# Kernel tuning notes

Hardware: AMD Instinct MI355X
Metric: run time of the kernel (lower is better)

The kernel has to match this reference:

```python
import jax, jax.numpy as jnp
import numpy as np
from jax.ops import segment_sum, segment_max, segment_min

N_NODES = 200000
N_HE = 100000     # number of hyperedges (nets)
NNZ = 1000000     # number of pins (node,hyperedge) incidences
F_RAW = 29        # raw node features; +2 fake_pos +1 ismacro = 32 = num_features
PIN_D = 4
C = 64            # nhid (heads = 1)
N_MACRO = 512
NUM_CLASSES = 1
SLOPE = 0.1


def _lrelu(v):
    return jnp.where(v >= 0, v, SLOPE * v)


def setup_inputs() -> dict:
    key = jax.random.key(0)
    ks = jax.random.split(key, 16)
    x = jax.random.normal(ks[0], (N_NODES, F_RAW), jnp.float32)
    fake_pos = jax.random.uniform(ks[1], (N_NODES, 2), dtype=jnp.float32)
    node_idx = jax.random.randint(ks[2], (NNZ,), 0, N_NODES)
    he_idx = jax.random.randint(ks[3], (NNZ,), 0, N_HE)
    edge_index = jnp.stack([node_idx, he_idx]).astype(jnp.int32)
    pin_feature = jax.random.normal(ks[4], (NNZ, PIN_D), jnp.float32)
    macro_index = jax.random.randint(ks[5], (N_MACRO,), 0, N_NODES).astype(jnp.int32)
    F_IN = F_RAW + 3

    def lin(k, fi, fo):
        return (jax.random.normal(k, (fi, fo), jnp.float32) / np.float32(np.sqrt(fi)))

    W1 = lin(ks[6], F_IN, C); b1 = jnp.zeros((C,), jnp.float32)
    Wpin = lin(ks[7], PIN_D, C)
    att = jax.random.normal(ks[8], (2 * C,), jnp.float32) / np.float32(np.sqrt(2 * C))
    Wpost = lin(ks[9], 4 * C, C); bpost = jnp.zeros((C,), jnp.float32)
    Wm1 = lin(ks[10], 2 * C, C); bm1 = jnp.zeros((C,), jnp.float32)
    Wm2 = lin(ks[11], C, C // 2); bm2 = jnp.zeros((C // 2,), jnp.float32)
    Wm3 = lin(ks[12], C // 2, NUM_CLASSES); bm3 = jnp.zeros((NUM_CLASSES,), jnp.float32)
    return dict(x=x, fake_pos=fake_pos, edge_index=edge_index, pin_feature=pin_feature,
                macro_index=macro_index, W1=W1, b1=b1, Wpin=Wpin, att=att,
                Wpost=Wpost, bpost=bpost, Wm1=Wm1, bm1=bm1, Wm2=Wm2, bm2=bm2,
                Wm3=Wm3, bm3=bm3)


def _forward(x, fake_pos, edge_index, pin_feature, macro_index,
             W1, b1, Wpin, att, Wpost, bpost, Wm1, bm1, Wm2, bm2, Wm3, bm3):
    node_idx = edge_index[0]
    he_idx = edge_index[1]

    ismacro = jnp.zeros((N_NODES, 1), x.dtype).at[macro_index].set(1.0)
    h = jnp.concatenate([x, fake_pos, ismacro], axis=-1)  # (N, 32)

    xl = h @ W1 + b1                                      # (N, C) node embedding
    pin_m = pin_feature @ Wpin                            # (NNZ, C) pin embedding

    # node -> hyperedge aggregation (mean over incident pins)
    msg_ne = xl[node_idx] + pin_m                         # (NNZ, C)
    deg_e = segment_sum(jnp.ones((NNZ,), x.dtype), he_idx, num_segments=N_HE)
    e_feat = segment_sum(msg_ne, he_idx, num_segments=N_HE) / jnp.maximum(deg_e, 1.0)[:, None]

    # attention over incident hyperedges, softmax per node
    e_g = e_feat[he_idx]                                  # (NNZ, C)
    a_raw = _lrelu(jnp.concatenate([xl[node_idx], e_g], axis=-1) @ att)  # (NNZ,)
    m = segment_max(a_raw, node_idx, num_segments=N_NODES)
    m = jnp.where(jnp.isfinite(m), m, 0.0)
    ex = jnp.exp(a_raw - m[node_idx])
    den = segment_sum(ex, node_idx, num_segments=N_NODES)
    alpha = ex / (den[node_idx] + 1e-16)

    # hyperedge -> node: PNA multi-aggregation of attention-weighted messages
    msg = e_g * alpha[:, None]                            # (NNZ, C)
    deg_n = segment_sum(jnp.ones((NNZ,), x.dtype), node_idx, num_segments=N_NODES)
    deg_c = jnp.maximum(deg_n, 1.0)[:, None]
    s = segment_sum(msg, node_idx, num_segments=N_NODES)
    mean = s / deg_c
    mx = segment_max(msg, node_idx, num_segments=N_NODES)
    mx = jnp.where(deg_n[:, None] > 0, mx, 0.0)
    mn = segment_min(msg, node_idx, num_segments=N_NODES)
    mn = jnp.where(deg_n[:, None] > 0, mn, 0.0)
    sq = segment_sum(msg * msg, node_idx, num_segments=N_NODES) / deg_c
    std = jnp.sqrt(jnp.maximum(sq - mean * mean, 0.0) + 1e-12)

    pna = jnp.concatenate([mean, mx, mn, std], axis=-1) @ Wpost + bpost  # (N, C)
    hx = _lrelu(pna)

    # masked global-mean pools (single graph: batch is all zeros)
    pooled = jnp.concatenate([hx[macro_index].mean(0), hx.mean(0)])[None, :]  # (1, 2C)

    z = _lrelu(pooled @ Wm1 + bm1)
    z = _lrelu(z @ Wm2 + bm2)
    return z @ Wm3 + bm3                                  # (1, num_classes)


def reference(x, fake_pos, edge_index, pin_feature, macro_index,
              W1, b1, Wpin, att, Wpost, bpost, Wm1, bm1, Wm2, bm2, Wm3, bm3):
    return _forward(x, fake_pos, edge_index, pin_feature, macro_index,
                    W1, b1, Wpin, att, Wpost, bpost, Wm1, bm1, Wm2, bm2, Wm3, bm3)
```

## Files before the change

### kernel.cpp

```cpp
#include <hip/hip_runtime.h>
#include <math.h>

#define N_NODES 200000
#define N_HE    100000
#define NNZ     1000000
#define F_RAW   29
#define N_MACRO 512
#define SLOPE   0.1f
#define L_TOTAL (N_NODES + N_HE)
#define NB_SCAN 293

typedef __attribute__((ext_vector_type(8))) short bf16x8;
typedef __attribute__((ext_vector_type(4))) float f32x4;

__device__ __forceinline__ float lrelu(float v) { return v >= 0.f ? v : SLOPE * v; }
__device__ __forceinline__ float bf2f(unsigned short u) { return __uint_as_float(((unsigned)u) << 16); }
__device__ __forceinline__ unsigned short f2bf(float f) {
    unsigned u = __float_as_uint(f);
    unsigned r = u + 0x7FFFu + ((u >> 16) & 1u);
    return (unsigned short)(r >> 16);
}
__device__ __forceinline__ float bflo(unsigned u) { return __uint_as_float(u << 16); }
__device__ __forceinline__ float bfhi(unsigned u) { return __uint_as_float(u & 0xffff0000u); }

__global__ __launch_bounds__(256) void fill_f32(float* p, long long n, float v) {
    long long i = (long long)blockIdx.x * blockDim.x + threadIdx.x;
    long long st = (long long)gridDim.x * blockDim.x;
    for (; i < n; i += st) p[i] = v;
}

__global__ __launch_bounds__(256) void k_pre(
    const int* __restrict__ mi, float* __restrict__ ismacro, int* __restrict__ mcount,
    const float* __restrict__ W1, const float* __restrict__ b1,
    const float* __restrict__ att, float* __restrict__ va,
    const int* __restrict__ nidx, const int* __restrict__ hidx,
    int* __restrict__ cnt, int* __restrict__ rank_n, int* __restrict__ rank_e)
{
    if (blockIdx.x == 0) {
        int t = threadIdx.x;
        if (t < 32) {
            float a = 0.f;
            for (int c = 0; c < 64; c++) a += W1[t * 64 + c] * att[c];
            va[t] = a;
        } else if (t == 32) {
            float a = 0.f;
            for (int c = 0; c < 64; c++) a += b1[c] * att[c];
            va[32] = a;
        }
    } else if (blockIdx.x <= 2) {
        int i = (blockIdx.x - 1) * 256 + threadIdx.x;
        if (i < N_MACRO) {
            ismacro[mi[i]] = 1.0f;
            atomicAdd(&mcount[mi[i]], 1);
        }
    } else {
        int i = (blockIdx.x - 3) * 256 + threadIdx.x;
        int st = (gridDim.x - 3) * 256;
        for (int p = i; p < NNZ; p += st) {
            rank_n[p] = atomicAdd(&cnt[nidx[p]], 1);
            rank_e[p] = atomicAdd(&cnt[N_NODES + hidx[p]], 1);
        }
    }
}

__global__ __launch_bounds__(256) void k_scan1(const int* __restrict__ cnt,
                                               int* __restrict__ row_ptr, int* __restrict__ partials)
{
    __shared__ int sA[256], sB[256];
    const int t = threadIdx.x;
    const int base = blockIdx.x * 1024 + t * 4;
    int v0 = base + 0 < L_TOTAL ? cnt[base + 0] : 0;
    int v1 = base + 1 < L_TOTAL ? cnt[base + 1] : 0;
    int v2 = base + 2 < L_TOTAL ? cnt[base + 2] : 0;
    int v3 = base + 3 < L_TOTAL ? cnt[base + 3] : 0;
    sA[t] = v0 + v1 + v2 + v3;
    __syncthreads();
    int* src = sA; int* dst = sB;
    for (int off = 1; off < 256; off <<= 1) {
        int v = src[t];
        if (t >= off) v += src[t - off];
        dst[t] = v;
        __syncthreads();
        int* tmp = src; src = dst; dst = tmp;
    }
    int excl = t > 0 ? src[t - 1] : 0;
    if (base + 0 < L_TOTAL) row_ptr[base + 0] = excl;
    if (base + 1 < L_TOTAL) row_ptr[base + 1] = excl + v0;
    if (base + 2 < L_TOTAL) row_ptr[base + 2] = excl + v0 + v1;
    if (base + 3 < L_TOTAL) row_ptr[base + 3] = excl + v0 + v1 + v2;
    if (t == 255) partials[blockIdx.x] = src[255];
}

__global__ __launch_bounds__(512) void k_scan2(int* __restrict__ partials)
{
    __shared__ int sA[512], sB[512];
    const int t = threadIdx.x;
    sA[t] = t < NB_SCAN ? partials[t] : 0;
    __syncthreads();
    int* src = sA; int* dst = sB;
    for (int off = 1; off < 512; off <<= 1) {
        int v = src[t];
        if (t >= off) v += src[t - off];
        dst[t] = v;
        __syncthreads();
        int* tmp = src; src = dst; dst = tmp;
    }
    if (t < NB_SCAN) partials[t] = t > 0 ? src[t - 1] : 0;
    if (t == 0) partials[NB_SCAN] = src[511];
}

__global__ __launch_bounds__(256) void k_scan3(int* __restrict__ row_ptr, const int* __restrict__ partials)
{
    const int base = blockIdx.x * 1024 + threadIdx.x * 4;
    int add = partials[blockIdx.x];
    #pragma unroll
    for (int k = 0; k < 4; k++)
        if (base + k < L_TOTAL) row_ptr[base + k] += add;
    if (blockIdx.x == 0 && threadIdx.x == 0) row_ptr[L_TOTAL] = partials[NB_SCAN];
}

__global__ __launch_bounds__(256) void k_mid(
    const int* __restrict__ nidx, const int* __restrict__ hidx,
    const int* __restrict__ row_ptr,
    const int* __restrict__ rank_n, const int* __restrict__ rank_e,
    const float4* __restrict__ pf4, int* __restrict__ csr_n, int4* __restrict__ rec,
    const float* __restrict__ x, const float* __restrict__ fp,
    const float* __restrict__ ismacro, const float* __restrict__ va,
    unsigned short* __restrict__ h, float* __restrict__ xn_att)
{
    if (blockIdx.x < 2048) {
        int i = blockIdx.x * 256 + threadIdx.x;
        int st = 2048 * 256;
        for (int p = i; p < NNZ; p += st) {
            int n = nidx[p], e = hidx[p];
            csr_n[row_ptr[n] + rank_n[p]] = e;
            int pe = row_ptr[N_NODES + e] + rank_e[p];
            float4 q = pf4[p];
            int4 r;
            r.x = n;
            r.y = (int)((unsigned)f2bf(q.x) | ((unsigned)f2bf(q.y) << 16));
            r.z = (int)((unsigned)f2bf(q.z) | ((unsigned)f2bf(q.w) << 16));
            r.w = 0;
            rec[pe - NNZ] = r;
        }
    } else {
        const int lane = threadIdx.x & 63;
        const int half = lane >> 5, k = lane & 31;
        int wid = ((blockIdx.x - 2048) * 256 + threadIdx.x) >> 6;
        int nw = (1024 * 256) >> 6;
        float vak = va[k];
        float c0 = va[32];
        for (int base = wid * 2; base < N_NODES; base += nw * 2) {
            int n = base + half;
            float v;
            if (k < 29)       v = x[(size_t)n * F_RAW + k];
            else if (k == 29) v = fp[2 * n];
            else if (k == 30) v = fp[2 * n + 1];
            else              v = ismacro[n];
            h[(size_t)n * 32 + k] = f2bf(v);
            float r = v * vak;
            #pragma unroll
            for (int o = 16; o > 0; o >>= 1) r += __shfl_xor(r, o, 32);
            if (k == 0) xn_att[n] = r + c0;
        }
    }
}

__global__ __launch_bounds__(256) void k_he_agg(
    const int* __restrict__ row_ptr, const int4* __restrict__ rec,
    const float* __restrict__ W1, const float* __restrict__ Wpin,
    const float* __restrict__ b1, const float* __restrict__ att,
    const unsigned short* __restrict__ h,
    unsigned short* __restrict__ e_feat, float* __restrict__ e_att)
{
    __shared__ float sW1[32 * 64];
    __shared__ float sWp[4 * 64];
    __shared__ float sb1[64];
    for (int i = threadIdx.x; i < 32 * 64; i += 256) sW1[i] = W1[i];
    for (int i = threadIdx.x; i < 4 * 64; i += 256) sWp[i] = Wpin[i];
    if (threadIdx.x < 64) sb1[threadIdx.x] = b1[threadIdx.x];
    __syncthreads();
    const int lane = threadIdx.x & 63;
    const int g  = lane >> 3;
    const int gl = lane & 7;
    float att2 = att[64 + lane];
    int wid = (blockIdx.x * blockDim.x + threadIdx.x) >> 6;
    int nw = (gridDim.x * blockDim.x) >> 6;
    for (int e = wid; e < N_HE; e += nw) {
        int start = row_ptr[N_NODES + e];
        int deg = row_ptr[N_NODES + e + 1] - start;
        float h0 = 0.f, h1 = 0.f, h2 = 0.f, h3 = 0.f;
        float pa = 0.f, pb = 0.f;
        const int4* rbase = rec + (start - NNZ);
        int t = g;
        for (; t + 8 < deg; t += 16) {
            int4 rA = rbase[t];
            int4 rB = rbase[t + 8];
            ushort4 uA = *(const ushort4*)&h[(size_t)rA.x * 32 + 4 * gl];
            ushort4 uB = *(const ushort4*)&h[(size_t)rB.x * 32 + 4 * gl];
            h0 += bf2f(uA.x) + bf2f(uB.x);
            h1 += bf2f(uA.y) + bf2f(uB.y);
            h2 += bf2f(uA.z) + bf2f(uB.z);
            h3 += bf2f(uA.w) + bf2f(uB.w);
            unsigned pyA = (gl == 0) ? (unsigned)rA.y : ((gl == 1) ? (unsigned)rA.z : 0u);
            unsigned pyB = (gl == 0) ? (unsigned)rB.y : ((gl == 1) ? (unsigned)rB.z : 0u);
            pa += bflo(pyA) + bflo(pyB);
            pb += bfhi(pyA) + bfhi(pyB);
        }
        if (t < deg) {
            int4 r = rbase[t];
            ushort4 u = *(const ushort4*)&h[(size_t)r.x * 32 + 4 * gl];
            h0 += bf2f(u.x); h1 += bf2f(u.y); h2 += bf2f(u.z); h3 += bf2f(u.w);
            unsigned py = (gl == 0) ? (unsigned)r.y : ((gl == 1) ? (unsigned)r.z : 0u);
            pa += bflo(py); pb += bfhi(py);
        }
        #pragma unroll
        for (int o = 8; o <= 32; o <<= 1) {
            h0 += __shfl_xor(h0, o); h1 += __shfl_xor(h1, o);
            h2 += __shfl_xor(h2, o); h3 += __shfl_xor(h3, o);
            pa += __shfl_xor(pa, o); pb += __shfl_xor(pb, o);
        }
        float p0 = __shfl(pa, 0, 64), p1 = __shfl(pb, 0, 64);
        float p2 = __shfl(pa, 1, 64), p3 = __shfl(pb, 1, 64);
        float acc = (float)deg * sb1[lane]
                  + p0 * sWp[lane] + p1 * sWp[64 + lane]
                  + p2 * sWp[128 + lane] + p3 * sWp[192 + lane];
        #pragma unroll
        for (int kk = 0; kk < 8; kk++) {
            float a0 = __shfl(h0, kk, 64), a1 = __shfl(h1, kk, 64);
            float a2 = __shfl(h2, kk, 64), a3 = __shfl(h3, kk, 64);
            acc += a0 * sW1[(4 * kk + 0) * 64 + lane] + a1 * sW1[(4 * kk + 1) * 64 + lane]
                 + a2 * sW1[(4 * kk + 2) * 64 + lane] + a3 * sW1[(4 * kk + 3) * 64 + lane];
        }
        float d = (float)(deg > 0 ? deg : 1);
        float v = acc / d;
        e_feat[(size_t)e * 64 + lane] = f2bf(v);
        float r = v * att2;
        #pragma unroll
        for (int o = 32; o > 0; o >>= 1) r += __shfl_down(r, o, 64);
        if (lane == 0) e_att[e] = r;
    }
}

__global__ __launch_bounds__(256, 4) void k_fused(
    const int* __restrict__ row_ptr, const int* __restrict__ csr,
    const float* __restrict__ xn_att, const float* __restrict__ e_att,
    const unsigned short* __restrict__ e_feat,
    const float* __restrict__ Wpost, const float* __restrict__ bpost,
    const int* __restrict__ mcount,
    float* __restrict__ sum_all, float* __restrict__ sum_mac)
{
    __shared__ __align__(16) unsigned short scat[16 * 264];
    const int lane = threadIdx.x & 63;
    const int wave = threadIdx.x >> 6;
    const int half = lane >> 5;
    const int c2   = lane & 31;
    const int quad = lane >> 4;
    const int nn   = lane & 15;
    bf16x8 wfrag[8];
    #pragma unroll
    for (int s = 0; s < 8; s++) {
        bf16x8 w;
        #pragma unroll
        for (int j = 0; j < 8; j++)
            w[j] = (short)f2bf(Wpost[(size_t)(32 * s + quad * 8 + j) * 64 + wave * 16 + nn]);
        wfrag[s] = w;
    }
    float bias = bpost[wave * 16 + nn];
    float pool = 0.f, pmac = 0.f;
    const int nbatches = N_NODES / 16;
    for (int b = blockIdx.x; b < nbatches; b += gridDim.x) {
        const int base = b * 16;
        __syncthreads();
        for (int i = 0; i < 4; i++) {
            int j = wave * 4 + i;
            int n = base + j;
            int start = row_ptr[n];
            int deg = row_ptr[n + 1] - start;
            float xn = xn_att[n];
            float sw = 0.f;
            float sx = 0.f, sy = 0.f, qx = 0.f, qy = 0.f;
            float mxx = -INFINITY, mxy = -INFINITY, mnx = INFINITY, mny = INFINITY;
            int t = half;
            for (; t + 2 < deg; t += 4) {
                int e0 = csr[start + t];
                int e1 = csr[start + t + 2];
                float w0 = __expf(lrelu(xn + e_att[e0]));
                float w1 = __expf(lrelu(xn + e_att[e1]));
                unsigned u0 = ((const unsigned*)&e_feat[(size_t)e0 * 64])[c2];
                unsigned u1 = ((const unsigned*)&e_feat[(size_t)e1 * 64])[c2];
                float v0x = bflo(u0) * w0, v0y = bfhi(u0) * w0;
                float v1x = bflo(u1) * w1, v1y = bfhi(u1) * w1;
                sw += w0 + w1;
                sx += v0x + v1x; sy += v0y + v1y;
                qx += v0x * v0x + v1x * v1x; qy += v0y * v0y + v1y * v1y;
                mxx = fmaxf(mxx, fmaxf(v0x, v1x)); mxy = fmaxf(mxy, fmaxf(v0y, v1y));
                mnx = fminf(mnx, fminf(v0x, v1x)); mny = fminf(mny, fminf(v0y, v1y));
            }
            for (; t < deg; t += 2) {
                int e = csr[start + t];
                float w = __expf(lrelu(xn + e_att[e]));
                unsigned u = ((const unsigned*)&e_feat[(size_t)e * 64])[c2];
                float vx = bflo(u) * w, vy = bfhi(u) * w;
                sw += w; sx += vx; sy += vy; qx += vx * vx; qy += vy * vy;
                mxx = fmaxf(mxx, vx); mxy = fmaxf(mxy, vy);
                mnx = fminf(mnx, vx); mny = fminf(mny, vy);
            }
            sw  += __shfl_xor(sw, 32);
            sx  += __shfl_xor(sx, 32);  sy += __shfl_xor(sy, 32);
            qx  += __shfl_xor(qx, 32);  qy += __shfl_xor(qy, 32);
            mxx = fmaxf(mxx, __shfl_xor(mxx, 32)); mxy = fmaxf(mxy, __shfl_xor(mxy, 32));
            mnx = fminf(mnx, __shfl_xor(mnx, 32)); mny = fminf(mny, __shfl_xor(mny, 32));
            float invD = 1.f / (sw + 1e-16f);
            float dc = (float)(deg > 0 ? deg : 1);
            float meanx = sx * invD / dc, meany = sy * invD / dc;
            float sqmx = qx * invD * invD / dc, sqmy = qy * invD * invD / dc;
            float stdx = sqrtf(fmaxf(sqmx - meanx * meanx, 0.f) + 1e-12f);
            float stdy = sqrtf(fmaxf(sqmy - meany * meany, 0.f) + 1e-12f);
            ushort2* row = (ushort2*)&scat[j * 264];
            if (half == 0) {
                ushort2 a; a.x = f2bf(meanx); a.y = f2bf(meany);
                row[c2] = a;
                ushort2 bmax; bmax.x = f2bf(deg > 0 ? mxx * invD : 0.f);
                bmax.y = f2bf(deg > 0 ? mxy * invD : 0.f);
                row[32 + c2] = bmax;
            } else {
                ushort2 bmin; bmin.x = f2bf(deg > 0 ? mnx * invD : 0.f);
                bmin.y = f2bf(deg > 0 ? mny * invD : 0.f);
                row[64 + c2] = bmin;
                ushort2 bstd; bstd.x = f2bf(stdx); bstd.y = f2bf(stdy);
                row[96 + c2] = bstd;
            }
        }
        __syncthreads();
        f32x4 acc = {0.f, 0.f, 0.f, 0.f};
        #pragma unroll
        for (int s = 0; s < 8; s++) {
            bf16x8 a = *(const bf16x8*)&scat[nn * 264 + 32 * s + quad * 8];
            acc = __builtin_amdgcn_mfma_f32_16x16x32_bf16(a, wfrag[s], acc, 0, 0, 0);
        }
        int4 mc4 = *(const int4*)&mcount[base + 4 * quad];
        float h0 = lrelu(acc[0] + bias);
        float h1 = lrelu(acc[1] + bias);
        float h2 = lrelu(acc[2] + bias);
        float h3 = lrelu(acc[3] + bias);
        pool += h0 + h1 + h2 + h3;
        pmac += (float)mc4.x * h0 + (float)mc4.y * h1 + (float)mc4.z * h2 + (float)mc4.w * h3;
    }
    pool += __shfl_xor(pool, 16); pool += __shfl_xor(pool, 32);
    pmac += __shfl_xor(pmac, 16); pmac += __shfl_xor(pmac, 32);
    if (quad == 0) {
        atomicAdd(&sum_all[wave * 16 + nn], pool);
        atomicAdd(&sum_mac[wave * 16 + nn], pmac);
    }
}

__global__ __launch_bounds__(256) void k_final(
    const float* __restrict__ sum_all, const float* __restrict__ sum_mac,
    const float* __restrict__ Wm1, const float* __restrict__ bm1,
    const float* __restrict__ Wm2, const float* __restrict__ bm2,
    const float* __restrict__ Wm3, const float* __restrict__ bm3,
    float* __restrict__ out)
{
    __shared__ float spool[128];
    __shared__ float z1[64];
    __shared__ float z2[32];
    if (threadIdx.x < 64) {
        spool[threadIdx.x]      = sum_mac[threadIdx.x] / (float)N_MACRO;
        spool[64 + threadIdx.x] = sum_all[threadIdx.x] / (float)N_NODES;
    }
    __syncthreads();
    if (threadIdx.x < 64) {
        int j = threadIdx.x;
        float a = bm1[j];
        #pragma unroll 4
        for (int k = 0; k < 128; k++) a += spool[k] * Wm1[k * 64 + j];
        z1[j] = lrelu(a);
    }
    __syncthreads();
    if (threadIdx.x < 32) {
        int j = threadIdx.x;
        float a = bm2[j];
        #pragma unroll 4
        for (int k = 0; k < 64; k++) a += z1[k] * Wm2[k * 32 + j];
        z2[j] = lrelu(a);
    }
    __syncthreads();
    if (threadIdx.x == 0) {
        float a = bm3[0];
        #pragma unroll
        for (int k = 0; k < 32; k++) a += z2[k] * Wm3[k];
        out[0] = a;
    }
}

extern "C" void kernel_launch(void* const* d_in, const int* in_sizes, int n_in,
                              void* d_out, int out_size, void* d_ws, size_t ws_size,
                              hipStream_t stream)
{
    const float* x        = (const float*)d_in[0];
    const float* fake_pos = (const float*)d_in[1];
    const int*   edge     = (const int*)d_in[2];
    const float* pinf     = (const float*)d_in[3];
    const int*   macro    = (const int*)d_in[4];
    const float* W1    = (const float*)d_in[5];
    const float* b1    = (const float*)d_in[6];
    const float* Wpin  = (const float*)d_in[7];
    const float* att   = (const float*)d_in[8];
    const float* Wpost = (const float*)d_in[9];
    const float* bpost = (const float*)d_in[10];
    const float* Wm1   = (const float*)d_in[11];
    const float* bm1   = (const float*)d_in[12];
    const float* Wm2   = (const float*)d_in[13];
    const float* bm2   = (const float*)d_in[14];
    const float* Wm3   = (const float*)d_in[15];
    const float* bm3   = (const float*)d_in[16];
    float* out = (float*)d_out;

    float* ws = (float*)d_ws;
    float*    ismacro = ws;
    float*    sum_all = ws + 200000;
    float*    sum_mac = ws + 200064;
    int*      mcount  = (int*)(ws + 200128);
    int*      cnt     = (int*)(ws + 400128);
    int*      row_ptr  = (int*)(ws + 700128);
    int*      partials = (int*)(ws + 1000132);
    float*    va       = ws + 1000432;
    int*      rank_n   = (int*)(ws + 1000472);
    int*      rank_e   = (int*)(ws + 2000472);
    int*      csr_n    = (int*)(ws + 3000472);
    int4*     rec      = (int4*)(ws + 4000472);
    float*    e_att    = ws + 8000472;
    float*    xn_att   = ws + 8100472;
    unsigned short* h      = (unsigned short*)(ws + 8300472);
    unsigned short* e_feat = (unsigned short*)(ws + 11500472);

    const int* nidx = edge;
    const int* hidx = edge + NNZ;

    fill_f32<<<1024, 256, 0, stream>>>(ws, 700128LL, 0.f);
    k_pre<<<2051, 256, 0, stream>>>(macro, ismacro, mcount, W1, b1, att, va,
                                    nidx, hidx, cnt, rank_n, rank_e);
    k_scan1<<<NB_SCAN, 256, 0, stream>>>(cnt, row_ptr, partials);
    k_scan2<<<1, 512, 0, stream>>>(partials);
    k_scan3<<<NB_SCAN, 256, 0, stream>>>(row_ptr, partials);
    k_mid<<<3072, 256, 0, stream>>>(nidx, hidx, row_ptr, rank_n, rank_e,
                                    (const float4*)pinf, csr_n, rec,
                                    x, fake_pos, ismacro, va, h, xn_att);
    k_he_agg<<<2048, 256, 0, stream>>>(row_ptr, rec, W1, Wpin, b1, att, h, e_feat, e_att);
    k_fused<<<2048, 256, 0, stream>>>(row_ptr, csr_n, xn_att, e_att, e_feat, Wpost, bpost,
                                      mcount, sum_all, sum_mac);
    k_final<<<1, 256, 0, stream>>>(sum_all, sum_mac, Wm1, bm1, Wm2, bm2, Wm3, bm3, out);
}
```

Before: 474.0 us.

## Precompute per-pin attention weights and move h-build into the counting kernel

Adds a k_wt pass that computes each node-pin attention weight and the per-node softmax denominator once, storing (edge, weight) pairs. k_fused then reads these pairs instead of recomputing the exp per lane and gathering e_att. The h/xn_att build moves from the scatter kernel into the atomic counting kernel, so it overlaps with the atomics instead of the scatter. In exchange, k_wt is a one-thread-per-node serial loop with extra writes of an 8 MB wrec array.

```diff
diff --git a/kernel.cpp b/kernel.cpp
--- a/kernel.cpp
+++ b/kernel.cpp
@@ -29,12 +29,10 @@
     for (; i < n; i += st) p[i] = v;
 }
 
-__global__ __launch_bounds__(256) void k_pre(
+__global__ __launch_bounds__(256) void k_tiny(
     const int* __restrict__ mi, float* __restrict__ ismacro, int* __restrict__ mcount,
     const float* __restrict__ W1, const float* __restrict__ b1,
-    const float* __restrict__ att, float* __restrict__ va,
-    const int* __restrict__ nidx, const int* __restrict__ hidx,
-    int* __restrict__ cnt, int* __restrict__ rank_n, int* __restrict__ rank_e)
+    const float* __restrict__ att, float* __restrict__ va)
 {
     if (blockIdx.x == 0) {
         int t = threadIdx.x;
@@ -47,83 +45,18 @@
             for (int c = 0; c < 64; c++) a += b1[c] * att[c];
             va[32] = a;
         }
-    } else if (blockIdx.x <= 2) {
+    } else {
         int i = (blockIdx.x - 1) * 256 + threadIdx.x;
         if (i < N_MACRO) {
             ismacro[mi[i]] = 1.0f;
             atomicAdd(&mcount[mi[i]], 1);
         }
-    } else {
-        int i = (blockIdx.x - 3) * 256 + threadIdx.x;
-        int st = (gridDim.x - 3) * 256;
-        for (int p = i; p < NNZ; p += st) {
-            rank_n[p] = atomicAdd(&cnt[nidx[p]], 1);
-            rank_e[p] = atomicAdd(&cnt[N_NODES + hidx[p]], 1);
-        }
-    }
-}
-
-__global__ __launch_bounds__(256) void k_scan1(const int* __restrict__ cnt,
-                                               int* __restrict__ row_ptr, int* __restrict__ partials)
-{
-    __shared__ int sA[256], sB[256];
-    const int t = threadIdx.x;
-    const int base = blockIdx.x * 1024 + t * 4;
-    int v0 = base + 0 < L_TOTAL ? cnt[base + 0] : 0;
-    int v1 = base + 1 < L_TOTAL ? cnt[base + 1] : 0;
-    int v2 = base + 2 < L_TOTAL ? cnt[base + 2] : 0;
-    int v3 = base + 3 < L_TOTAL ? cnt[base + 3] : 0;
-    sA[t] = v0 + v1 + v2 + v3;
-    __syncthreads();
-    int* src = sA; int* dst = sB;
-    for (int off = 1; off < 256; off <<= 1) {
-        int v = src[t];
-        if (t >= off) v += src[t - off];
-        dst[t] = v;
-        __syncthreads();
-        int* tmp = src; src = dst; dst = tmp;
-    }
-    int excl = t > 0 ? src[t - 1] : 0;
-    if (base + 0 < L_TOTAL) row_ptr[base + 0] = excl;
-    if (base + 1 < L_TOTAL) row_ptr[base + 1] = excl + v0;
-    if (base + 2 < L_TOTAL) row_ptr[base + 2] = excl + v0 + v1;
-    if (base + 3 < L_TOTAL) row_ptr[base + 3] = excl + v0 + v1 + v2;
-    if (t == 255) partials[blockIdx.x] = src[255];
-}
-
-__global__ __launch_bounds__(512) void k_scan2(int* __restrict__ partials)
-{
-    __shared__ int sA[512], sB[512];
-    const int t = threadIdx.x;
-    sA[t] = t < NB_SCAN ? partials[t] : 0;
-    __syncthreads();
-    int* src = sA; int* dst = sB;
-    for (int off = 1; off < 512; off <<= 1) {
-        int v = src[t];
-        if (t >= off) v += src[t - off];
-        dst[t] = v;
-        __syncthreads();
-        int* tmp = src; src = dst; dst = tmp;
-    }
-    if (t < NB_SCAN) partials[t] = t > 0 ? src[t - 1] : 0;
-    if (t == 0) partials[NB_SCAN] = src[511];
-}
-
-__global__ __launch_bounds__(256) void k_scan3(int* __restrict__ row_ptr, const int* __restrict__ partials)
-{
-    const int base = blockIdx.x * 1024 + threadIdx.x * 4;
-    int add = partials[blockIdx.x];
-    #pragma unroll
-    for (int k = 0; k < 4; k++)
-        if (base + k < L_TOTAL) row_ptr[base + k] += add;
-    if (blockIdx.x == 0 && threadIdx.x == 0) row_ptr[L_TOTAL] = partials[NB_SCAN];
-}
-
-__global__ __launch_bounds__(256) void k_mid(
+    }
+}
+
+__global__ __launch_bounds__(256) void k_cnt_h(
     const int* __restrict__ nidx, const int* __restrict__ hidx,
-    const int* __restrict__ row_ptr,
-    const int* __restrict__ rank_n, const int* __restrict__ rank_e,
-    const float4* __restrict__ pf4, int* __restrict__ csr_n, int4* __restrict__ rec,
+    int* __restrict__ cnt, int* __restrict__ rank_n, int* __restrict__ rank_e,
     const float* __restrict__ x, const float* __restrict__ fp,
     const float* __restrict__ ismacro, const float* __restrict__ va,
     unsigned short* __restrict__ h, float* __restrict__ xn_att)
@@ -132,16 +65,8 @@
         int i = blockIdx.x * 256 + threadIdx.x;
         int st = 2048 * 256;
         for (int p = i; p < NNZ; p += st) {
-            int n = nidx[p], e = hidx[p];
-            csr_n[row_ptr[n] + rank_n[p]] = e;
-            int pe = row_ptr[N_NODES + e] + rank_e[p];
-            float4 q = pf4[p];
-            int4 r;
-            r.x = n;
-            r.y = (int)((unsigned)f2bf(q.x) | ((unsigned)f2bf(q.y) << 16));
-            r.z = (int)((unsigned)f2bf(q.z) | ((unsigned)f2bf(q.w) << 16));
-            r.w = 0;
-            rec[pe - NNZ] = r;
+            rank_n[p] = atomicAdd(&cnt[nidx[p]], 1);
+            rank_e[p] = atomicAdd(&cnt[N_NODES + hidx[p]], 1);
         }
     } else {
         const int lane = threadIdx.x & 63;
@@ -163,6 +88,84 @@
             for (int o = 16; o > 0; o >>= 1) r += __shfl_xor(r, o, 32);
             if (k == 0) xn_att[n] = r + c0;
         }
+    }
+}
+
+__global__ __launch_bounds__(256) void k_scan1(const int* __restrict__ cnt,
+                                               int* __restrict__ row_ptr, int* __restrict__ partials)
+{
+    __shared__ int sA[256], sB[256];
+    const int t = threadIdx.x;
+    const int base = blockIdx.x * 1024 + t * 4;
+    int v0 = base + 0 < L_TOTAL ? cnt[base + 0] : 0;
+    int v1 = base + 1 < L_TOTAL ? cnt[base + 1] : 0;
+    int v2 = base + 2 < L_TOTAL ? cnt[base + 2] : 0;
+    int v3 = base + 3 < L_TOTAL ? cnt[base + 3] : 0;
+    sA[t] = v0 + v1 + v2 + v3;
+    __syncthreads();
+    int* src = sA; int* dst = sB;
+    for (int off = 1; off < 256; off <<= 1) {
+        int v = src[t];
+        if (t >= off) v += src[t - off];
+        dst[t] = v;
+        __syncthreads();
+        int* tmp = src; src = dst; dst = tmp;
+    }
+    int excl = t > 0 ? src[t - 1] : 0;
+    if (base + 0 < L_TOTAL) row_ptr[base + 0] = excl;
+    if (base + 1 < L_TOTAL) row_ptr[base + 1] = excl + v0;
+    if (base + 2 < L_TOTAL) row_ptr[base + 2] = excl + v0 + v1;
+    if (base + 3 < L_TOTAL) row_ptr[base + 3] = excl + v0 + v1 + v2;
+    if (t == 255) partials[blockIdx.x] = src[255];
+}
+
+__global__ __launch_bounds__(512) void k_scan2(int* __restrict__ partials)
+{
+    __shared__ int sA[512], sB[512];
+    const int t = threadIdx.x;
+    sA[t] = t < NB_SCAN ? partials[t] : 0;
+    __syncthreads();
+    int* src = sA; int* dst = sB;
+    for (int off = 1; off < 512; off <<= 1) {
+        int v = src[t];
+        if (t >= off) v += src[t - off];
+        dst[t] = v;
+        __syncthreads();
+        int* tmp = src; src = dst; dst = tmp;
+    }
+    if (t < NB_SCAN) partials[t] = t > 0 ? src[t - 1] : 0;
+    if (t == 0) partials[NB_SCAN] = src[511];
+}
+
+__global__ __launch_bounds__(256) void k_scan3(int* __restrict__ row_ptr, const int* __restrict__ partials)
+{
+    const int base = blockIdx.x * 1024 + threadIdx.x * 4;
+    int add = partials[blockIdx.x];
+    #pragma unroll
+    for (int k = 0; k < 4; k++)
+        if (base + k < L_TOTAL) row_ptr[base + k] += add;
+    if (blockIdx.x == 0 && threadIdx.x == 0) row_ptr[L_TOTAL] = partials[NB_SCAN];
+}
+
+__global__ __launch_bounds__(256) void k_scatter(
+    const int* __restrict__ nidx, const int* __restrict__ hidx,
+    const int* __restrict__ row_ptr,
+    const int* __restrict__ rank_n, const int* __restrict__ rank_e,
+    const float4* __restrict__ pf4, int* __restrict__ csr_n, int4* __restrict__ rec)
+{
+    int i = blockIdx.x * 256 + threadIdx.x;
+    int st = gridDim.x * 256;
+    for (int p = i; p < NNZ; p += st) {
+        int n = nidx[p], e = hidx[p];
+        csr_n[row_ptr[n] + rank_n[p]] = e;
+        int pe = row_ptr[N_NODES + e] + rank_e[p];
+        float4 q = pf4[p];
+        int4 r;
+        r.x = n;
+        r.y = (int)((unsigned)f2bf(q.x) | ((unsigned)f2bf(q.y) << 16));
+        r.z = (int)((unsigned)f2bf(q.z) | ((unsigned)f2bf(q.w) << 16));
+        r.w = 0;
+        rec[pe - NNZ] = r;
     }
 }
 
@@ -242,9 +245,32 @@
     }
 }
 
+__global__ __launch_bounds__(256) void k_wt(
+    const int* __restrict__ row_ptr, const int* __restrict__ csr_n,
+    const float* __restrict__ xn_att, const float* __restrict__ e_att,
+    int2* __restrict__ wrec, float* __restrict__ inv_den)
+{
+    int i = blockIdx.x * 256 + threadIdx.x;
+    int st = gridDim.x * 256;
+    for (int n = i; n < N_NODES; n += st) {
+        int start = row_ptr[n];
+        int deg = row_ptr[n + 1] - start;
+        float xn = xn_att[n];
+        float sw = 0.f;
+        for (int t = 0; t < deg; t++) {
+            int e = csr_n[start + t];
+            float w = __expf(lrelu(xn + e_att[e]));
+            sw += w;
+            int2 r; r.x = e; r.y = __float_as_int(w);
+            wrec[start + t] = r;
+        }
+        inv_den[n] = 1.f / (sw + 1e-16f);
+    }
+}
+
 __global__ __launch_bounds__(256, 4) void k_fused(
-    const int* __restrict__ row_ptr, const int* __restrict__ csr,
-    const float* __restrict__ xn_att, const float* __restrict__ e_att,
+    const int* __restrict__ row_ptr, const int2* __restrict__ wrec,
+    const float* __restrict__ inv_den, const float* __restrict__ e_att,
     const unsigned short* __restrict__ e_feat,
     const float* __restrict__ Wpost, const float* __restrict__ bpost,
     const int* __restrict__ mcount,
@@ -277,41 +303,38 @@
             int n = base + j;
             int start = row_ptr[n];
             int deg = row_ptr[n + 1] - start;
-            float xn = xn_att[n];
-            float sw = 0.f;
+            const int2* rb = wrec + start;
             float sx = 0.f, sy = 0.f, qx = 0.f, qy = 0.f;
             float mxx = -INFINITY, mxy = -INFINITY, mnx = INFINITY, mny = INFINITY;
             int t = half;
             for (; t + 2 < deg; t += 4) {
-                int e0 = csr[start + t];
-                int e1 = csr[start + t + 2];
-                float w0 = __expf(lrelu(xn + e_att[e0]));
-                float w1 = __expf(lrelu(xn + e_att[e1]));
-                unsigned u0 = ((const unsigned*)&e_feat[(size_t)e0 * 64])[c2];
-                unsigned u1 = ((const unsigned*)&e_feat[(size_t)e1 * 64])[c2];
+                int2 r0 = rb[t];
+                int2 r1 = rb[t + 2];
+                float w0 = __int_as_float(r0.y);
+                float w1 = __int_as_float(r1.y);
+                unsigned u0 = ((const unsigned*)&e_feat[(size_t)r0.x * 64])[c2];
+                unsigned u1 = ((const unsigned*)&e_feat[(size_t)r1.x * 64])[c2];
                 float v0x = bflo(u0) * w0, v0y = bfhi(u0) * w0;
                 float v1x = bflo(u1) * w1, v1y = bfhi(u1) * w1;
-                sw += w0 + w1;
                 sx += v0x + v1x; sy += v0y + v1y;
                 qx += v0x * v0x + v1x * v1x; qy += v0y * v0y + v1y * v1y;
                 mxx = fmaxf(mxx, fmaxf(v0x, v1x)); mxy = fmaxf(mxy, fmaxf(v0y, v1y));
                 mnx = fminf(mnx, fminf(v0x, v1x)); mny = fminf(mny, fminf(v0y, v1y));
             }
             for (; t < deg; t += 2) {
-                int e = csr[start + t];
-                float w = __expf(lrelu(xn + e_att[e]));
-                unsigned u = ((const unsigned*)&e_feat[(size_t)e * 64])[c2];
+                int2 r = rb[t];
+                float w = __int_as_float(r.y);
+                unsigned u = ((const unsigned*)&e_feat[(size_t)r.x * 64])[c2];
                 float vx = bflo(u) * w, vy = bfhi(u) * w;
-                sw += w; sx += vx; sy += vy; qx += vx * vx; qy += vy * vy;
+                sx += vx; sy += vy; qx += vx * vx; qy += vy * vy;
                 mxx = fmaxf(mxx, vx); mxy = fmaxf(mxy, vy);
                 mnx = fminf(mnx, vx); mny = fminf(mny, vy);
             }
-            sw  += __shfl_xor(sw, 32);
             sx  += __shfl_xor(sx, 32);  sy += __shfl_xor(sy, 32);
             qx  += __shfl_xor(qx, 32);  qy += __shfl_xor(qy, 32);
             mxx = fmaxf(mxx, __shfl_xor(mxx, 32)); mxy = fmaxf(mxy, __shfl_xor(mxy, 32));
             mnx = fminf(mnx, __shfl_xor(mnx, 32)); mny = fminf(mny, __shfl_xor(mny, 32));
-            float invD = 1.f / (sw + 1e-16f);
+            float invD = inv_den[n];
             float dc = (float)(deg > 0 ? deg : 1);
             float meanx = sx * invD / dc, meany = sy * invD / dc;
             float sqmx = qx * invD * invD / dc, sqmy = qy * invD * invD / dc;
@@ -430,25 +453,28 @@
     int*      rank_e   = (int*)(ws + 2000472);
     int*      csr_n    = (int*)(ws + 3000472);
     int4*     rec      = (int4*)(ws + 4000472);
-    float*    e_att    = ws + 8000472;
-    float*    xn_att   = ws + 8100472;
-    unsigned short* h      = (unsigned short*)(ws + 8300472);
-    unsigned short* e_feat = (unsigned short*)(ws + 11500472);
+    int2*     wrec     = (int2*)(ws + 8000472);
+    float*    inv_den  = ws + 10000472;
+    float*    e_att    = ws + 10200472;
+    float*    xn_att   = ws + 10300472;
+    unsigned short* h      = (unsigned short*)(ws + 10500472);
+    unsigned short* e_feat = (unsigned short*)(ws + 13700472);
 
     const int* nidx = edge;
     const int* hidx = edge + NNZ;
 
     fill_f32<<<1024, 256, 0, stream>>>(ws, 700128LL, 0.f);
-    k_pre<<<2051, 256, 0, stream>>>(macro, ismacro, mcount, W1, b1, att, va,
-                                    nidx, hidx, cnt, rank_n, rank_e);
+    k_tiny<<<3, 256, 0, stream>>>(macro, ismacro, mcount, W1, b1, att, va);
+    k_cnt_h<<<3072, 256, 0, stream>>>(nidx, hidx, cnt, rank_n, rank_e,
+                                      x, fake_pos, ismacro, va, h, xn_att);
     k_scan1<<<NB_SCAN, 256, 0, stream>>>(cnt, row_ptr, partials);
     k_scan2<<<1, 512, 0, stream>>>(partials);
     k_scan3<<<NB_SCAN, 256, 0, stream>>>(row_ptr, partials);
-    k_mid<<<3072, 256, 0, stream>>>(nidx, hidx, row_ptr, rank_n, rank_e,
-                                    (const float4*)pinf, csr_n, rec,
-                                    x, fake_pos, ismacro, va, h, xn_att);
+    k_scatter<<<2048, 256, 0, stream>>>(nidx, hidx, row_ptr, rank_n, rank_e,
+                                        (const float4*)pinf, csr_n, rec);
     k_he_agg<<<2048, 256, 0, stream>>>(row_ptr, rec, W1, Wpin, b1, att, h, e_feat, e_att);
-    k_fused<<<2048, 256, 0, stream>>>(row_ptr, csr_n, xn_att, e_att, e_feat, Wpost, bpost,
+    k_wt<<<782, 256, 0, stream>>>(row_ptr, csr_n, xn_att, e_att, wrec, inv_den);
+    k_fused<<<2048, 256, 0, stream>>>(row_ptr, wrec, inv_den, e_att, e_feat, Wpost, bpost,
                                       mcount, sum_all, sum_mac);
     k_final<<<1, 256, 0, stream>>>(sum_all, sum_mac, Wm1, bm1, Wm2, bm2, Wm3, bm3, out);
 }
```

After: 489.6 us. 3.3% more time.

## Regroup counting with node-feature prep and widen per-lane gather in node aggregation

Applied to the files above, without the earlier changes.

The node-feature packing and attention-score computation move out of the post-scan scatter kernel and into the same launch as the atomic counting pass, so the scatter kernel only builds the CSR and record arrays. The ismacro and va setup is split into a tiny separate kernel that runs first, since the feature packing now depends on it. In the node aggregation, each lane now handles four feature channels across quarter-wave slices of the neighbour list instead of two channels across half-waves. This gives wider ushort4 loads and a direct 8-byte store into the shared staging tile, at the cost of more accumulator registers and a two-step shuffle reduction.

```diff
diff --git a/kernel.cpp b/kernel.cpp
--- a/kernel.cpp
+++ b/kernel.cpp
@@ -29,12 +29,10 @@
     for (; i < n; i += st) p[i] = v;
 }
 
-__global__ __launch_bounds__(256) void k_pre(
+__global__ __launch_bounds__(256) void k_tiny(
     const int* __restrict__ mi, float* __restrict__ ismacro, int* __restrict__ mcount,
     const float* __restrict__ W1, const float* __restrict__ b1,
-    const float* __restrict__ att, float* __restrict__ va,
-    const int* __restrict__ nidx, const int* __restrict__ hidx,
-    int* __restrict__ cnt, int* __restrict__ rank_n, int* __restrict__ rank_e)
+    const float* __restrict__ att, float* __restrict__ va)
 {
     if (blockIdx.x == 0) {
         int t = threadIdx.x;
@@ -47,83 +45,18 @@
             for (int c = 0; c < 64; c++) a += b1[c] * att[c];
             va[32] = a;
         }
-    } else if (blockIdx.x <= 2) {
+    } else {
         int i = (blockIdx.x - 1) * 256 + threadIdx.x;
         if (i < N_MACRO) {
             ismacro[mi[i]] = 1.0f;
             atomicAdd(&mcount[mi[i]], 1);
         }
-    } else {
-        int i = (blockIdx.x - 3) * 256 + threadIdx.x;
-        int st = (gridDim.x - 3) * 256;
-        for (int p = i; p < NNZ; p += st) {
-            rank_n[p] = atomicAdd(&cnt[nidx[p]], 1);
-            rank_e[p] = atomicAdd(&cnt[N_NODES + hidx[p]], 1);
-        }
-    }
-}
-
-__global__ __launch_bounds__(256) void k_scan1(const int* __restrict__ cnt,
-                                               int* __restrict__ row_ptr, int* __restrict__ partials)
-{
-    __shared__ int sA[256], sB[256];
-    const int t = threadIdx.x;
-    const int base = blockIdx.x * 1024 + t * 4;
-    int v0 = base + 0 < L_TOTAL ? cnt[base + 0] : 0;
-    int v1 = base + 1 < L_TOTAL ? cnt[base + 1] : 0;
-    int v2 = base + 2 < L_TOTAL ? cnt[base + 2] : 0;
-    int v3 = base + 3 < L_TOTAL ? cnt[base + 3] : 0;
-    sA[t] = v0 + v1 + v2 + v3;
-    __syncthreads();
-    int* src = sA; int* dst = sB;
-    for (int off = 1; off < 256; off <<= 1) {
-        int v = src[t];
-        if (t >= off) v += src[t - off];
-        dst[t] = v;
-        __syncthreads();
-        int* tmp = src; src = dst; dst = tmp;
-    }
-    int excl = t > 0 ? src[t - 1] : 0;
-    if (base + 0 < L_TOTAL) row_ptr[base + 0] = excl;
-    if (base + 1 < L_TOTAL) row_ptr[base + 1] = excl + v0;
-    if (base + 2 < L_TOTAL) row_ptr[base + 2] = excl + v0 + v1;
-    if (base + 3 < L_TOTAL) row_ptr[base + 3] = excl + v0 + v1 + v2;
-    if (t == 255) partials[blockIdx.x] = src[255];
-}
-
-__global__ __launch_bounds__(512) void k_scan2(int* __restrict__ partials)
-{
-    __shared__ int sA[512], sB[512];
-    const int t = threadIdx.x;
-    sA[t] = t < NB_SCAN ? partials[t] : 0;
-    __syncthreads();
-    int* src = sA; int* dst = sB;
-    for (int off = 1; off < 512; off <<= 1) {
-        int v = src[t];
-        if (t >= off) v += src[t - off];
-        dst[t] = v;
-        __syncthreads();
-        int* tmp = src; src = dst; dst = tmp;
-    }
-    if (t < NB_SCAN) partials[t] = t > 0 ? src[t - 1] : 0;
-    if (t == 0) partials[NB_SCAN] = src[511];
-}
-
-__global__ __launch_bounds__(256) void k_scan3(int* __restrict__ row_ptr, const int* __restrict__ partials)
-{
-    const int base = blockIdx.x * 1024 + threadIdx.x * 4;
-    int add = partials[blockIdx.x];
-    #pragma unroll
-    for (int k = 0; k < 4; k++)
-        if (base + k < L_TOTAL) row_ptr[base + k] += add;
-    if (blockIdx.x == 0 && threadIdx.x == 0) row_ptr[L_TOTAL] = partials[NB_SCAN];
-}
-
-__global__ __launch_bounds__(256) void k_mid(
+    }
+}
+
+__global__ __launch_bounds__(256) void k_cnt_h(
     const int* __restrict__ nidx, const int* __restrict__ hidx,
-    const int* __restrict__ row_ptr,
-    const int* __restrict__ rank_n, const int* __restrict__ rank_e,
-    const float4* __restrict__ pf4, int* __restrict__ csr_n, int4* __restrict__ rec,
+    int* __restrict__ cnt, int* __restrict__ rank_n, int* __restrict__ rank_e,
     const float* __restrict__ x, const float* __restrict__ fp,
     const float* __restrict__ ismacro, const float* __restrict__ va,
     unsigned short* __restrict__ h, float* __restrict__ xn_att)
@@ -132,16 +65,8 @@
         int i = blockIdx.x * 256 + threadIdx.x;
         int st = 2048 * 256;
         for (int p = i; p < NNZ; p += st) {
-            int n = nidx[p], e = hidx[p];
-            csr_n[row_ptr[n] + rank_n[p]] = e;
-            int pe = row_ptr[N_NODES + e] + rank_e[p];
-            float4 q = pf4[p];
-            int4 r;
-            r.x = n;
-            r.y = (int)((unsigned)f2bf(q.x) | ((unsigned)f2bf(q.y) << 16));
-            r.z = (int)((unsigned)f2bf(q.z) | ((unsigned)f2bf(q.w) << 16));
-            r.w = 0;
-            rec[pe - NNZ] = r;
+            rank_n[p] = atomicAdd(&cnt[nidx[p]], 1);
+            rank_e[p] = atomicAdd(&cnt[N_NODES + hidx[p]], 1);
         }
     } else {
         const int lane = threadIdx.x & 63;
@@ -163,6 +88,84 @@
             for (int o = 16; o > 0; o >>= 1) r += __shfl_xor(r, o, 32);
             if (k == 0) xn_att[n] = r + c0;
         }
+    }
+}
+
+__global__ __launch_bounds__(256) void k_scan1(const int* __restrict__ cnt,
+                                               int* __restrict__ row_ptr, int* __restrict__ partials)
+{
+    __shared__ int sA[256], sB[256];
+    const int t = threadIdx.x;
+    const int base = blockIdx.x * 1024 + t * 4;
+    int v0 = base + 0 < L_TOTAL ? cnt[base + 0] : 0;
+    int v1 = base + 1 < L_TOTAL ? cnt[base + 1] : 0;
+    int v2 = base + 2 < L_TOTAL ? cnt[base + 2] : 0;
+    int v3 = base + 3 < L_TOTAL ? cnt[base + 3] : 0;
+    sA[t] = v0 + v1 + v2 + v3;
+    __syncthreads();
+    int* src = sA; int* dst = sB;
+    for (int off = 1; off < 256; off <<= 1) {
+        int v = src[t];
+        if (t >= off) v += src[t - off];
+        dst[t] = v;
+        __syncthreads();
+        int* tmp = src; src = dst; dst = tmp;
+    }
+    int excl = t > 0 ? src[t - 1] : 0;
+    if (base + 0 < L_TOTAL) row_ptr[base + 0] = excl;
+    if (base + 1 < L_TOTAL) row_ptr[base + 1] = excl + v0;
+    if (base + 2 < L_TOTAL) row_ptr[base + 2] = excl + v0 + v1;
+    if (base + 3 < L_TOTAL) row_ptr[base + 3] = excl + v0 + v1 + v2;
+    if (t == 255) partials[blockIdx.x] = src[255];
+}
+
+__global__ __launch_bounds__(512) void k_scan2(int* __restrict__ partials)
+{
+    __shared__ int sA[512], sB[512];
+    const int t = threadIdx.x;
+    sA[t] = t < NB_SCAN ? partials[t] : 0;
+    __syncthreads();
+    int* src = sA; int* dst = sB;
+    for (int off = 1; off < 512; off <<= 1) {
+        int v = src[t];
+        if (t >= off) v += src[t - off];
+        dst[t] = v;
+        __syncthreads();
+        int* tmp = src; src = dst; dst = tmp;
+    }
+    if (t < NB_SCAN) partials[t] = t > 0 ? src[t - 1] : 0;
+    if (t == 0) partials[NB_SCAN] = src[511];
+}
+
+__global__ __launch_bounds__(256) void k_scan3(int* __restrict__ row_ptr, const int* __restrict__ partials)
+{
+    const int base = blockIdx.x * 1024 + threadIdx.x * 4;
+    int add = partials[blockIdx.x];
+    #pragma unroll
+    for (int k = 0; k < 4; k++)
+        if (base + k < L_TOTAL) row_ptr[base + k] += add;
+    if (blockIdx.x == 0 && threadIdx.x == 0) row_ptr[L_TOTAL] = partials[NB_SCAN];
+}
+
+__global__ __launch_bounds__(256) void k_scatter(
+    const int* __restrict__ nidx, const int* __restrict__ hidx,
+    const int* __restrict__ row_ptr,
+    const int* __restrict__ rank_n, const int* __restrict__ rank_e,
+    const float4* __restrict__ pf4, int* __restrict__ csr_n, int4* __restrict__ rec)
+{
+    int i = blockIdx.x * 256 + threadIdx.x;
+    int st = gridDim.x * 256;
+    for (int p = i; p < NNZ; p += st) {
+        int n = nidx[p], e = hidx[p];
+        csr_n[row_ptr[n] + rank_n[p]] = e;
+        int pe = row_ptr[N_NODES + e] + rank_e[p];
+        float4 q = pf4[p];
+        int4 r;
+        r.x = n;
+        r.y = (int)((unsigned)f2bf(q.x) | ((unsigned)f2bf(q.y) << 16));
+        r.z = (int)((unsigned)f2bf(q.z) | ((unsigned)f2bf(q.w) << 16));
+        r.w = 0;
+        rec[pe - NNZ] = r;
     }
 }
 
@@ -253,8 +256,6 @@
     __shared__ __align__(16) unsigned short scat[16 * 264];
     const int lane = threadIdx.x & 63;
     const int wave = threadIdx.x >> 6;
-    const int half = lane >> 5;
-    const int c2   = lane & 31;
     const int quad = lane >> 4;
     const int nn   = lane & 15;
     bf16x8 wfrag[8];
@@ -279,58 +280,62 @@
             int deg = row_ptr[n + 1] - start;
             float xn = xn_att[n];
             float sw = 0.f;
-            float sx = 0.f, sy = 0.f, qx = 0.f, qy = 0.f;
-            float mxx = -INFINITY, mxy = -INFINITY, mnx = INFINITY, mny = INFINITY;
-            int t = half;
-            for (; t + 2 < deg; t += 4) {
-                int e0 = csr[start + t];
-                int e1 = csr[start + t + 2];
-                float w0 = __expf(lrelu(xn + e_att[e0]));
-                float w1 = __expf(lrelu(xn + e_att[e1]));
-                unsigned u0 = ((const unsigned*)&e_feat[(size_t)e0 * 64])[c2];
-                unsigned u1 = ((const unsigned*)&e_feat[(size_t)e1 * 64])[c2];
-                float v0x = bflo(u0) * w0, v0y = bfhi(u0) * w0;
-                float v1x = bflo(u1) * w1, v1y = bfhi(u1) * w1;
-                sw += w0 + w1;
-                sx += v0x + v1x; sy += v0y + v1y;
-                qx += v0x * v0x + v1x * v1x; qy += v0y * v0y + v1y * v1y;
-                mxx = fmaxf(mxx, fmaxf(v0x, v1x)); mxy = fmaxf(mxy, fmaxf(v0y, v1y));
-                mnx = fminf(mnx, fminf(v0x, v1x)); mny = fminf(mny, fminf(v0y, v1y));
-            }
-            for (; t < deg; t += 2) {
+            float s0 = 0.f, s1 = 0.f, s2 = 0.f, s3 = 0.f;
+            float q0 = 0.f, q1 = 0.f, q2 = 0.f, q3 = 0.f;
+            float mx0 = -INFINITY, mx1 = -INFINITY, mx2 = -INFINITY, mx3 = -INFINITY;
+            float mn0 = INFINITY, mn1 = INFINITY, mn2 = INFINITY, mn3 = INFINITY;
+            for (int t = quad; t < deg; t += 4) {
                 int e = csr[start + t];
                 float w = __expf(lrelu(xn + e_att[e]));
-                unsigned u = ((const unsigned*)&e_feat[(size_t)e * 64])[c2];
-                float vx = bflo(u) * w, vy = bfhi(u) * w;
-                sw += w; sx += vx; sy += vy; qx += vx * vx; qy += vy * vy;
-                mxx = fmaxf(mxx, vx); mxy = fmaxf(mxy, vy);
-                mnx = fminf(mnx, vx); mny = fminf(mny, vy);
+                ushort4 u = *(const ushort4*)&e_feat[(size_t)e * 64 + 4 * nn];
+                float v0 = bf2f(u.x) * w, v1 = bf2f(u.y) * w;
+                float v2 = bf2f(u.z) * w, v3 = bf2f(u.w) * w;
+                sw += w;
+                s0 += v0; s1 += v1; s2 += v2; s3 += v3;
+                q0 += v0 * v0; q1 += v1 * v1; q2 += v2 * v2; q3 += v3 * v3;
+                mx0 = fmaxf(mx0, v0); mx1 = fmaxf(mx1, v1);
+                mx2 = fmaxf(mx2, v2); mx3 = fmaxf(mx3, v3);
+                mn0 = fminf(mn0, v0); mn1 = fminf(mn1, v1);
+                mn2 = fminf(mn2, v2); mn3 = fminf(mn3, v3);
             }
-            sw  += __shfl_xor(sw, 32);
-            sx  += __shfl_xor(sx, 32);  sy += __shfl_xor(sy, 32);
-            qx  += __shfl_xor(qx, 32);  qy += __shfl_xor(qy, 32);
-            mxx = fmaxf(mxx, __shfl_xor(mxx, 32)); mxy = fmaxf(mxy, __shfl_xor(mxy, 32));
-            mnx = fminf(mnx, __shfl_xor(mnx, 32)); mny = fminf(mny, __shfl_xor(mny, 32));
+            #pragma unroll
+            for (int o = 16; o <= 32; o <<= 1) {
+                sw += __shfl_xor(sw, o);
+                s0 += __shfl_xor(s0, o); s1 += __shfl_xor(s1, o);
+                s2 += __shfl_xor(s2, o); s3 += __shfl_xor(s3, o);
+                q0 += __shfl_xor(q0, o); q1 += __shfl_xor(q1, o);
+                q2 += __shfl_xor(q2, o); q3 += __shfl_xor(q3, o);
+                mx0 = fmaxf(mx0, __shfl_xor(mx0, o)); mx1 = fmaxf(mx1, __shfl_xor(mx1, o));
+                mx2 = fmaxf(mx2, __shfl_xor(mx2, o)); mx3 = fmaxf(mx3, __shfl_xor(mx3, o));
+                mn0 = fminf(mn0, __shfl_xor(mn0, o)); mn1 = fminf(mn1, __shfl_xor(mn1, o));
+                mn2 = fminf(mn2, __shfl_xor(mn2, o)); mn3 = fminf(mn3, __shfl_xor(mn3, o));
+            }
             float invD = 1.f / (sw + 1e-16f);
             float dc = (float)(deg > 0 ? deg : 1);
-            float meanx = sx * invD / dc, meany = sy * invD / dc;
-            float sqmx = qx * invD * invD / dc, sqmy = qy * invD * invD / dc;
-            float stdx = sqrtf(fmaxf(sqmx - meanx * meanx, 0.f) + 1e-12f);
-            float stdy = sqrtf(fmaxf(sqmy - meany * meany, 0.f) + 1e-12f);
-            ushort2* row = (ushort2*)&scat[j * 264];
-            if (half == 0) {
-                ushort2 a; a.x = f2bf(meanx); a.y = f2bf(meany);
-                row[c2] = a;
-                ushort2 bmax; bmax.x = f2bf(deg > 0 ? mxx * invD : 0.f);
-                bmax.y = f2bf(deg > 0 ? mxy * invD : 0.f);
-                row[32 + c2] = bmax;
+            float idc = invD / dc;
+            float a0, a1, a2, a3;
+            if (quad == 0) {
+                a0 = s0 * idc; a1 = s1 * idc; a2 = s2 * idc; a3 = s3 * idc;
+            } else if (quad == 1) {
+                a0 = deg > 0 ? mx0 * invD : 0.f;
+                a1 = deg > 0 ? mx1 * invD : 0.f;
+                a2 = deg > 0 ? mx2 * invD : 0.f;
+                a3 = deg > 0 ? mx3 * invD : 0.f;
+            } else if (quad == 2) {
+                a0 = deg > 0 ? mn0 * invD : 0.f;
+                a1 = deg > 0 ? mn1 * invD : 0.f;
+                a2 = deg > 0 ? mn2 * invD : 0.f;
+                a3 = deg > 0 ? mn3 * invD : 0.f;
             } else {
-                ushort2 bmin; bmin.x = f2bf(deg > 0 ? mnx * invD : 0.f);
-                bmin.y = f2bf(deg > 0 ? mny * invD : 0.f);
-                row[64 + c2] = bmin;
-                ushort2 bstd; bstd.x = f2bf(stdx); bstd.y = f2bf(stdy);
-                row[96 + c2] = bstd;
+                float m0 = s0 * idc, m1 = s1 * idc, m2 = s2 * idc, m3 = s3 * idc;
+                a0 = sqrtf(fmaxf(q0 * invD * idc - m0 * m0, 0.f) + 1e-12f);
+                a1 = sqrtf(fmaxf(q1 * invD * idc - m1 * m1, 0.f) + 1e-12f);
+                a2 = sqrtf(fmaxf(q2 * invD * idc - m2 * m2, 0.f) + 1e-12f);
+                a3 = sqrtf(fmaxf(q3 * invD * idc - m3 * m3, 0.f) + 1e-12f);
             }
+            ushort4 o4;
+            o4.x = f2bf(a0); o4.y = f2bf(a1); o4.z = f2bf(a2); o4.w = f2bf(a3);
+            *(ushort4*)&scat[j * 264 + quad * 64 + 4 * nn] = o4;
         }
         __syncthreads();
         f32x4 acc = {0.f, 0.f, 0.f, 0.f};
@@ -439,14 +444,14 @@
     const int* hidx = edge + NNZ;
 
     fill_f32<<<1024, 256, 0, stream>>>(ws, 700128LL, 0.f);
-    k_pre<<<2051, 256, 0, stream>>>(macro, ismacro, mcount, W1, b1, att, va,
-                                    nidx, hidx, cnt, rank_n, rank_e);
+    k_tiny<<<3, 256, 0, stream>>>(macro, ismacro, mcount, W1, b1, att, va);
+    k_cnt_h<<<3072, 256, 0, stream>>>(nidx, hidx, cnt, rank_n, rank_e,
+                                      x, fake_pos, ismacro, va, h, xn_att);
     k_scan1<<<NB_SCAN, 256, 0, stream>>>(cnt, row_ptr, partials);
     k_scan2<<<1, 512, 0, stream>>>(partials);
     k_scan3<<<NB_SCAN, 256, 0, stream>>>(row_ptr, partials);
-    k_mid<<<3072, 256, 0, stream>>>(nidx, hidx, row_ptr, rank_n, rank_e,
-                                    (const float4*)pinf, csr_n, rec,
-                                    x, fake_pos, ismacro, va, h, xn_att);
+    k_scatter<<<2048, 256, 0, stream>>>(nidx, hidx, row_ptr, rank_n, rank_e,
+                                        (const float4*)pinf, csr_n, rec);
     k_he_agg<<<2048, 256, 0, stream>>>(row_ptr, rec, W1, Wpin, b1, att, h, e_feat, e_att);
     k_fused<<<2048, 256, 0, stream>>>(row_ptr, csr_n, xn_att, e_att, e_feat, Wpost, bpost,
                                       mcount, sum_all, sum_mac);
```

New measurement: 488.1 us. +3.0%, slower.
